# Kernel optimization log

Measured on AMD Instinct MI355X. Metric: run time of the kernel, lower is better.

## Reference

```python
import jax, jax.numpy as jnp
import numpy as np

J = 58        # n_joints (two 29-joint dancers)
NIN = 192     # n_in
H = 512       # n_hid
NOUT = 128    # n_out
B = 32        # batch


def _xavier(key, fan_in, fan_out):
    return jax.random.normal(key, (fan_in, fan_out), jnp.float32) * jnp.sqrt(2.0 / (fan_in + fan_out))


def setup_inputs() -> dict:
    key = jax.random.key(0)
    ks = jax.random.split(key, 8)
    # fully-connected directed graph, no self loops: E = J*(J-1) = 3306
    src_np, dst_np = np.nonzero(1 - np.eye(J, dtype=np.int32))
    edge_index = jnp.asarray(np.stack([src_np, dst_np]), dtype=jnp.int32)  # [2, E]
    x = jax.random.normal(ks[0], (B, 1, J, NIN), jnp.float32)
    return dict(
        x=x,
        edge_index=edge_index,
        gcn1_w=_xavier(ks[1], NIN, H), gcn1_b=jnp.full((H,), 0.1, jnp.float32),
        mlp1_w=_xavier(ks[2], 2 * H, H), mlp1_b=jnp.full((H,), 0.1, jnp.float32),
        bn1_g=jnp.ones((H,), jnp.float32), bn1_b=jnp.zeros((H,), jnp.float32),
        gcn2_w=_xavier(ks[3], H, H), gcn2_b=jnp.full((H,), 0.1, jnp.float32),
        mlp2_w=_xavier(ks[4], 3 * H, H), mlp2_b=jnp.full((H,), 0.1, jnp.float32),
        bn2_g=jnp.ones((H,), jnp.float32), bn2_b=jnp.zeros((H,), jnp.float32),
        fc_w=_xavier(ks[5], H, NOUT), fc_b=jnp.full((NOUT,), 0.1, jnp.float32),
    )


def _gcn_norm_adj(edge_index, n_nodes, dtype):
    # PyG GCNConv default: A_hat = A + I, sym-normalized D^-1/2 A_hat D^-1/2
    src, dst = edge_index[0], edge_index[1]
    adj = jnp.zeros((n_nodes, n_nodes), dtype).at[dst, src].add(1.0) + jnp.eye(n_nodes, dtype=dtype)
    d_inv_sqrt = 1.0 / jnp.sqrt(adj.sum(axis=1))
    return d_inv_sqrt[:, None] * adj * d_inv_sqrt[None, :]


def _batchnorm(h, gamma, beta):
    # BatchNorm1d (training-mode stats) over (batch, length) per channel
    mu = h.mean(axis=(0, 1))
    var = h.var(axis=(0, 1))
    return (h - mu) * jax.lax.rsqrt(var + 1e-5) * gamma + beta


def reference(x, edge_index, gcn1_w, gcn1_b, mlp1_w, mlp1_b, bn1_g, bn1_b,
              gcn2_w, gcn2_b, mlp2_w, mlp2_b, bn2_g, bn2_b, fc_w, fc_b):
    b = x.shape[0]
    n = x.shape[2]
    x = x.reshape(b, n, -1)                                  # [B, J, n_in]
    src, dst = edge_index[0], edge_index[1]
    A = _gcn_norm_adj(edge_index, n, x.dtype)                # [J, J]

    # GCNConv 1 + relu
    h = jax.nn.relu(jnp.einsum('ij,bjf->bif', A, x) @ gcn1_w + gcn1_b)   # [B, J, H]
    # node2edge: concat(sender, receiver) feats -> MLP1 -> BN (batched gather)
    e = jnp.concatenate([h[:, src], h[:, dst]], axis=-1)     # [B, E, 2H]
    e = jax.nn.relu(e @ mlp1_w + mlp1_b)                     # [B, E, H]
    e = _batchnorm(e, bn1_g, bn1_b)                          # dropout p=0 -> identity
    x_skip = e
    # edge2node: sum incoming edge feats per receiver node (m_in^T @ e)
    node = jnp.zeros((b, n, e.shape[-1]), e.dtype).at[:, dst].add(e)     # [B, J, H]

    # GCNConv 2 + relu
    h2 = jax.nn.relu(jnp.einsum('ij,bjf->bif', A, node) @ gcn2_w + gcn2_b)
    # node2edge again, concat skip, MLP2, BN, fc_out
    e2 = jnp.concatenate([h2[:, src], h2[:, dst], x_skip], axis=-1)      # [B, E, 3H]
    e2 = jax.nn.relu(e2 @ mlp2_w + mlp2_b)
    e2 = _batchnorm(e2, bn2_g, bn2_b)
    return e2 @ fc_w + fc_b                                  # [B, E, n_out]
```

## Files before the change

kernel.cpp:

```cpp
#include <hip/hip_runtime.h>
#include <stdint.h>

#define J_ 58
#define E_ 3306
#define B_ 32
#define NIN_ 192
#define H_ 512
#define NOUT_ 128
#define M_EDGE (B_*E_)
#define M_PAD  (M_EDGE + 64)
#define M_NODE (B_*J_)
#define NSLOT 64

typedef unsigned short u16;
typedef __attribute__((ext_vector_type(8))) short short8v;
typedef __attribute__((ext_vector_type(4))) float f32x4;

__device__ __forceinline__ float b2f(u16 u){ return __uint_as_float(((uint32_t)u)<<16); }
__device__ __forceinline__ u16 f2b(float f){
  uint32_t u = __float_as_uint(f);
  u += 0x7FFFu + ((u>>16)&1u);
  return (u16)(u>>16);
}
__device__ __forceinline__ void async16(const void* g, void* l){
  __builtin_amdgcn_global_load_lds((const __attribute__((address_space(1))) uint32_t*)g,
                                   (__attribute__((address_space(3))) uint32_t*)l, 16, 0, 0);
}

__global__ __launch_bounds__(256) void build_graph(const int* __restrict__ ei,
    float* __restrict__ Adj, float* __restrict__ aind,
    int* __restrict__ csroff, int* __restrict__ csredg)
{
  __shared__ float adj[J_][J_];
  __shared__ int   deg[J_];
  __shared__ float dinv[J_];
  __shared__ int   off[J_+1];
  __shared__ int   cur[J_];
  const int t = threadIdx.x;
  const int* srcI = ei;
  const int* dstI = ei + E_;
  for (int i = t; i < J_*J_; i += 256) adj[i/J_][i%J_] = 0.f;
  if (t < J_) { deg[t] = 0; cur[t] = 0; }
  __syncthreads();
  for (int e = t; e < E_; e += 256) {
    atomicAdd(&adj[dstI[e]][srcI[e]], 1.f);
    atomicAdd(&deg[dstI[e]], 1);
  }
  __syncthreads();
  if (t < J_) adj[t][t] += 1.f;
  __syncthreads();
  if (t < J_) {
    float s = 0.f;
    for (int j = 0; j < J_; ++j) s += adj[t][j];
    dinv[t] = rsqrtf(s);
  }
  __syncthreads();
  for (int i = t; i < J_*J_; i += 256) {
    int r = i / J_, c = i % J_;
    Adj[i] = dinv[r]*adj[r][c]*dinv[c];
  }
  if (t < J_) {
    float s = 0.f;
    for (int j = 0; j < J_; ++j) s += dinv[t]*adj[t][j]*dinv[j]*(float)deg[j];
    aind[t] = s;
  }
  if (t == 0) {
    off[0] = 0;
    for (int n = 0; n < J_; ++n) off[n+1] = off[n] + deg[n];
  }
  __syncthreads();
  if (t <= J_) csroff[t] = off[t];
  for (int e = t; e < E_; e += 256) {
    int d = dstI[e];
    int p = atomicAdd(&cur[d], 1);
    csredg[off[d] + p] = e;
  }
}

__global__ __launch_bounds__(256) void transpose_cv(const float* __restrict__ src,
    u16* __restrict__ dst, int K, int N)
{
  int idx = blockIdx.x*256 + threadIdx.x;
  if (idx >= K*N) return;
  int k = idx / N, n = idx - k*N;
  dst[(size_t)n*K + k] = f2b(src[idx]);
}

__global__ __launch_bounds__(192) void ax_kernel(const float* __restrict__ Adj,
    const float* __restrict__ x, u16* __restrict__ Ax)
{
  int bi = blockIdx.x;
  int b = bi / J_, i = bi - b*J_;
  __shared__ float Arow[J_];
  if (threadIdx.x < J_) Arow[threadIdx.x] = Adj[i*J_ + threadIdx.x];
  __syncthreads();
  int f = threadIdx.x;
  const float* xb = x + (size_t)b*J_*NIN_ + f;
  float acc = 0.f;
  for (int j = 0; j < J_; ++j) acc += Arow[j]*xb[(size_t)j*NIN_];
  Ax[(size_t)bi*NIN_ + f] = f2b(acc);
}

template<int MODE>
__global__ __launch_bounds__(256) void gemm64(
    const u16* __restrict__ Aop, const u16* __restrict__ Bt,
    const int M, const int N, const int K,
    const float* __restrict__ bias,
    u16* __restrict__ outB, float* __restrict__ outF)
{
  __shared__ __align__(16) u16 Al[64*32];
  __shared__ __align__(16) u16 Bl[64*32];
  const int tid = threadIdx.x;
  const int w = tid >> 6, l = tid & 63;
  const int row0 = blockIdx.x * 64, col0 = blockIdx.y * 64;
  f32x4 acc[4] = {};
  const u16* ag = Aop + (size_t)(row0 + (tid>>2))*K + (tid&3)*8;
  const u16* bg = Bt  + (size_t)(col0 + (tid>>2))*K + (tid&3)*8;
  const int fr = l & 15, fg = l >> 4;
  const int nk = K >> 5;
  for (int kt = 0; kt < nk; ++kt) {
    short8v av = *(const short8v*)ag;
    short8v bv = *(const short8v*)bg;
    ag += 32; bg += 32;
    __syncthreads();
    *(short8v*)(Al + tid*8) = av;
    *(short8v*)(Bl + tid*8) = bv;
    __syncthreads();
    short8v a = *(const short8v*)(Al + (w*16 + fr)*32 + fg*8);
#pragma unroll
    for (int nt = 0; nt < 4; ++nt) {
      short8v b = *(const short8v*)(Bl + (nt*16 + fr)*32 + fg*8);
      acc[nt] = __builtin_amdgcn_mfma_f32_16x16x32_bf16(a, b, acc[nt], 0, 0, 0);
    }
  }
#pragma unroll
  for (int nt = 0; nt < 4; ++nt) {
    int gc = col0 + nt*16 + fr;
    float bv = (MODE == 1) ? bias[gc] : 0.f;
#pragma unroll
    for (int r = 0; r < 4; ++r) {
      int gr = row0 + w*16 + fg*4 + r;
      if (MODE == 0) outF[(size_t)gr*N + gc] = acc[nt][r];
      else           outB[(size_t)gr*N + gc] = f2b(fmaxf(acc[nt][r] + bv, 0.f));
    }
  }
}

template<int MODE>
__global__ __launch_bounds__(256, 3) void gemm128(
    const u16* __restrict__ Aop, const u16* __restrict__ Bt,
    const int N, const int K,
    const float* __restrict__ g1, const float* __restrict__ g2,
    const float* __restrict__ crow,
    const int* __restrict__ srcI, const int* __restrict__ dstI,
    double* __restrict__ sumslot, double* __restrict__ sqslot,
    u16* __restrict__ outB, float* __restrict__ outF)
{
  __shared__ __align__(16) u16 Al[2][128*32];
  __shared__ __align__(16) u16 Bl[2][128*32];
  const int tid = threadIdx.x;
  const int w = tid >> 6, l = tid & 63;
  const int wm = w >> 1, wn = w & 1;
  const int row0 = blockIdx.x * 128, col0 = blockIdx.y * 128;
  const int fr = l & 15, fg = l >> 4;
  f32x4 acc[4][4] = {};
  const int srow = l >> 2, skoff = (l & 3) * 8;
  const u16* agA = Aop + (size_t)(row0 + w*16 + srow)*K + skoff;
  const u16* agB = Bt  + (size_t)(col0 + w*16 + srow)*K + skoff;
  const size_t rstep = (size_t)64 * K;
  const int nk = K >> 5;
  async16(agA,         &Al[0][w*512]);
  async16(agA + rstep, &Al[0][2048 + w*512]);
  async16(agB,         &Bl[0][w*512]);
  async16(agB + rstep, &Bl[0][2048 + w*512]);
  __syncthreads();
  for (int kt = 0; kt < nk; ++kt) {
    const int cur = kt & 1, nxt = cur ^ 1;
    if (kt + 1 < nk) {
      const u16* pa = agA + (kt+1)*32;
      const u16* pb = agB + (kt+1)*32;
      async16(pa,         &Al[nxt][w*512]);
      async16(pa + rstep, &Al[nxt][2048 + w*512]);
      async16(pb,         &Bl[nxt][w*512]);
      async16(pb + rstep, &Bl[nxt][2048 + w*512]);
    }
    short8v a[4], b[4];
#pragma unroll
    for (int i = 0; i < 4; ++i)
      a[i] = *(const short8v*)(&Al[cur][(wm*64 + i*16 + fr)*32 + fg*8]);
#pragma unroll
    for (int j = 0; j < 4; ++j)
      b[j] = *(const short8v*)(&Bl[cur][(wn*64 + j*16 + fr)*32 + fg*8]);
#pragma unroll
    for (int i = 0; i < 4; ++i)
#pragma unroll
      for (int j = 0; j < 4; ++j)
        acc[i][j] = __builtin_amdgcn_mfma_f32_16x16x32_bf16(a[i], b[j], acc[i][j], 0, 0, 0);
    __syncthreads();
  }

  if (MODE == 2) {
    int mr[4][4];
    uint32_t off1[4][4], off2[4][4];
#pragma unroll
    for (int i = 0; i < 4; ++i)
#pragma unroll
      for (int r = 0; r < 4; ++r) {
        int m = row0 + wm*64 + i*16 + fg*4 + r;
        mr[i][r] = m;
        int mm = (m < M_EDGE) ? m : 0;
        uint32_t bb = (uint32_t)mm / E_;
        uint32_t ke = (uint32_t)mm - bb*E_;
        off1[i][r] = (bb*J_ + (uint32_t)srcI[ke])*H_;
        off2[i][r] = (bb*J_ + (uint32_t)dstI[ke])*H_;
      }
    const int slot = blockIdx.x & (NSLOT-1);
#pragma unroll
    for (int j = 0; j < 4; ++j) {
      int gc = col0 + wn*64 + j*16 + fr;
      float cr = crow[gc];
      double s = 0.0, q = 0.0;
#pragma unroll
      for (int i = 0; i < 4; ++i)
#pragma unroll
        for (int r = 0; r < 4; ++r) {
          float v = acc[i][j][r] + g1[off1[i][r] + gc] + g2[off2[i][r] + gc] + cr;
          v = fmaxf(v, 0.f);
          if (mr[i][r] < M_EDGE) {
            outB[(size_t)mr[i][r]*N + gc] = f2b(v);
            double vd = (double)v;
            s += vd; q += vd*vd;
          }
        }
      s += __shfl_xor(s, 16); s += __shfl_xor(s, 32);
      q += __shfl_xor(q, 16); q += __shfl_xor(q, 32);
      if (fg == 0) {
        atomicAdd(&sumslot[(size_t)slot*H_ + gc], s);
        atomicAdd(&sqslot [(size_t)slot*H_ + gc], q);
      }
    }
  } else {
#pragma unroll
    for (int j = 0; j < 4; ++j) {
      int gc = col0 + wn*64 + j*16 + fr;
      float cr = crow[gc];
#pragma unroll
      for (int i = 0; i < 4; ++i)
#pragma unroll
        for (int r = 0; r < 4; ++r) {
          int m = row0 + wm*64 + i*16 + fg*4 + r;
          if (m < M_EDGE) outF[(size_t)m*N + gc] = acc[i][j][r] + cr;
        }
    }
  }
}

__global__ __launch_bounds__(256) void edge1_kernel(const float* __restrict__ hs,
    const float* __restrict__ hd, const float* __restrict__ b1,
    const int* __restrict__ srcI, const int* __restrict__ dstI,
    u16* __restrict__ e_raw, double* __restrict__ sumslot, double* __restrict__ sqslot)
{
  const int t = threadIdx.x;
  const int row0 = blockIdx.x * 16;
  float bv0 = b1[t], bv1 = b1[t+256];
  double s0=0.0,q0=0.0,s1=0.0,q1=0.0;
  for (int r = 0; r < 16; ++r) {
    int m = row0 + r;
    uint32_t bb = (uint32_t)m / E_;
    uint32_t ke = (uint32_t)m - bb*E_;
    const float* ps = hs + ((size_t)bb*J_ + srcI[ke])*H_;
    const float* pd = hd + ((size_t)bb*J_ + dstI[ke])*H_;
    float v0 = fmaxf(ps[t]     + pd[t]     + bv0, 0.f);
    float v1 = fmaxf(ps[t+256] + pd[t+256] + bv1, 0.f);
    e_raw[(size_t)m*H_ + t]       = f2b(v0);
    e_raw[(size_t)m*H_ + t + 256] = f2b(v1);
    double d0 = (double)v0, d1 = (double)v1;
    s0 += d0; q0 += d0*d0; s1 += d1; q1 += d1*d1;
  }
  const int slot = blockIdx.x & (NSLOT-1);
  atomicAdd(&sumslot[(size_t)slot*H_ + t],     s0);
  atomicAdd(&sumslot[(size_t)slot*H_ + t+256], s1);
  atomicAdd(&sqslot [(size_t)slot*H_ + t],     q0);
  atomicAdd(&sqslot [(size_t)slot*H_ + t+256], q1);
}

__global__ __launch_bounds__(512) void bn_fin(const double* __restrict__ sumslot,
    const double* __restrict__ sqslot, const float* __restrict__ g, const float* __restrict__ b,
    float* __restrict__ scale, float* __restrict__ shift)
{
  int c = threadIdx.x;
  double s = 0.0, q = 0.0;
  for (int k = 0; k < NSLOT; ++k) { s += sumslot[(size_t)k*H_ + c]; q += sqslot[(size_t)k*H_ + c]; }
  const double invM = 1.0 / (double)M_EDGE;
  double mu = s * invM;
  double var = q * invM - mu*mu;
  if (var < 0.0) var = 0.0;
  float sc = g[c] * (float)(1.0 / sqrt(var + 1e-5));
  scale[c] = sc;
  shift[c] = b[c] - (float)mu*sc;
}

__global__ __launch_bounds__(256) void build_wc(const float* __restrict__ m2w,
    const float* __restrict__ m2b, const float* __restrict__ scale1, const float* __restrict__ shift1,
    u16* __restrict__ WcT, float* __restrict__ crow)
{
  int n = blockIdx.x;
  int t = threadIdx.x;
  __shared__ float red[256];
  float part = 0.f;
  for (int k = t; k < H_; k += 256) {
    float wv = m2w[(size_t)(2*H_ + k)*H_ + n];
    WcT[(size_t)n*H_ + k] = f2b(scale1[k]*wv);
    part += shift1[k]*wv;
  }
  red[t] = part; __syncthreads();
  for (int s = 128; s; s >>= 1) { if (t < s) red[t] += red[t+s]; __syncthreads(); }
  if (t == 0) crow[n] = red[0] + m2b[n];
}

__global__ __launch_bounds__(256) void build_fc(const float* __restrict__ fcw,
    const float* __restrict__ fcb, const float* __restrict__ scale2, const float* __restrict__ shift2,
    u16* __restrict__ fcT, float* __restrict__ cvec)
{
  int n = blockIdx.x;
  int t = threadIdx.x;
  __shared__ float red[256];
  float part = 0.f;
  for (int k = t; k < H_; k += 256) {
    float wv = fcw[(size_t)k*NOUT_ + n];
    fcT[(size_t)n*H_ + k] = f2b(scale2[k]*wv);
    part += shift2[k]*wv;
  }
  red[t] = part; __syncthreads();
  for (int s = 128; s; s >>= 1) { if (t < s) red[t] += red[t+s]; __syncthreads(); }
  if (t == 0) cvec[n] = red[0] + fcb[n];
}

__global__ __launch_bounds__(256) void scatter_kernel(const u16* __restrict__ e_raw,
    const int* __restrict__ csroff, const int* __restrict__ csredg, float* __restrict__ node_raw)
{
  int bi = blockIdx.x;
  int b = bi / J_, n = bi - b*J_;
  int beg = csroff[n], end = csroff[n+1];
  int c0 = threadIdx.x, c1 = threadIdx.x + 256;
  float a0 = 0.f, a1 = 0.f;
  for (int p = beg; p < end; ++p) {
    const u16* er = e_raw + ((size_t)b*E_ + csredg[p])*H_;
    a0 += b2f(er[c0]); a1 += b2f(er[c1]);
  }
  node_raw[(size_t)bi*H_ + c0] = a0;
  node_raw[(size_t)bi*H_ + c1] = a1;
}

__global__ __launch_bounds__(256) void an_kernel(const float* __restrict__ Adj,
    const float* __restrict__ node_raw, const float* __restrict__ scale1,
    const float* __restrict__ shift1, const float* __restrict__ aind, u16* __restrict__ An)
{
  int bi = blockIdx.x;
  int b = bi / J_, i = bi - b*J_;
  __shared__ float Arow[J_];
  if (threadIdx.x < J_) Arow[threadIdx.x] = Adj[i*J_ + threadIdx.x];
  __syncthreads();
  float ai = aind[i];
#pragma unroll
  for (int h = 0; h < 2; ++h) {
    int c = threadIdx.x + h*256;
    const float* nb = node_raw + (size_t)b*J_*H_ + c;
    float acc = 0.f;
    for (int j = 0; j < J_; ++j) acc += Arow[j]*nb[(size_t)j*H_];
    An[(size_t)bi*H_ + c] = f2b(scale1[c]*acc + shift1[c]*ai);
  }
}

extern "C" void kernel_launch(void* const* d_in, const int* in_sizes, int n_in,
                              void* d_out, int out_size, void* d_ws, size_t ws_size,
                              hipStream_t stream)
{
  const float* x    = (const float*)d_in[0];
  const int*   ei   = (const int*)d_in[1];
  const float* g1w  = (const float*)d_in[2];
  const float* g1b  = (const float*)d_in[3];
  const float* m1w  = (const float*)d_in[4];
  const float* m1b  = (const float*)d_in[5];
  const float* bn1g = (const float*)d_in[6];
  const float* bn1b = (const float*)d_in[7];
  const float* g2w  = (const float*)d_in[8];
  const float* g2b  = (const float*)d_in[9];
  const float* m2w  = (const float*)d_in[10];
  const float* m2b  = (const float*)d_in[11];
  const float* bn2g = (const float*)d_in[12];
  const float* bn2b = (const float*)d_in[13];
  const float* fcw  = (const float*)d_in[14];
  const float* fcb  = (const float*)d_in[15];

  char* wsp = (char*)d_ws;
  size_t off = 0;
  auto alloc = [&](size_t bytes) -> char* {
    char* p = wsp + off;
    off = (off + bytes + 255) & ~(size_t)255;
    return p;
  };
  float* Adj    = (float*)alloc(J_*J_*4);
  float* aind   = (float*)alloc(J_*4);
  int*   csroff = (int*)alloc((J_+1)*4);
  int*   csredg = (int*)alloc(E_*4);
  float* scale1 = (float*)alloc(H_*4);
  float* shift1 = (float*)alloc(H_*4);
  float* scale2 = (float*)alloc(H_*4);
  float* shift2 = (float*)alloc(H_*4);
  float* crow1  = (float*)alloc(H_*4);
  float* cvec   = (float*)alloc(NOUT_*4);
  double* slots = (double*)alloc((size_t)4*NSLOT*H_*8);
  double* sum1 = slots;
  double* sq1  = slots + (size_t)NSLOT*H_;
  double* sum2 = slots + (size_t)2*NSLOT*H_;
  double* sq2  = slots + (size_t)3*NSLOT*H_;
  u16* g1T  = (u16*)alloc((size_t)H_*NIN_*2);
  u16* g2T  = (u16*)alloc((size_t)H_*H_*2);
  u16* W1aT = (u16*)alloc((size_t)H_*H_*2);
  u16* W1bT = (u16*)alloc((size_t)H_*H_*2);
  u16* W2aT = (u16*)alloc((size_t)H_*H_*2);
  u16* W2bT = (u16*)alloc((size_t)H_*H_*2);
  u16* WcT  = (u16*)alloc((size_t)H_*H_*2);
  u16* fcT  = (u16*)alloc((size_t)NOUT_*H_*2);
  u16* Ax   = (u16*)alloc((size_t)M_NODE*NIN_*2);
  u16* h    = (u16*)alloc((size_t)M_NODE*H_*2);
  float* hs = (float*)alloc((size_t)M_NODE*H_*4);
  float* hd = (float*)alloc((size_t)M_NODE*H_*4);
  float* node_raw = (float*)alloc((size_t)M_NODE*H_*4);
  u16* An   = (u16*)alloc((size_t)M_NODE*H_*2);
  u16* h2   = (u16*)alloc((size_t)M_NODE*H_*2);
  float* h2s = (float*)alloc((size_t)M_NODE*H_*4);
  float* h2d = (float*)alloc((size_t)M_NODE*H_*4);
  u16* e_raw = (u16*)alloc((size_t)M_PAD*H_*2);
  u16* e2    = (u16*)alloc((size_t)M_PAD*H_*2);
  if (off > ws_size) return;

  const int* srcI = ei;
  const int* dstI = ei + E_;
  float* outF = (float*)d_out;

  hipMemsetAsync(slots, 0, (size_t)4*NSLOT*H_*8, stream);
  build_graph<<<1, 256, 0, stream>>>(ei, Adj, aind, csroff, csredg);

  transpose_cv<<<(NIN_*H_+255)/256, 256, 0, stream>>>(g1w, g1T, NIN_, H_);
  transpose_cv<<<(H_*H_+255)/256, 256, 0, stream>>>(g2w, g2T, H_, H_);
  transpose_cv<<<(H_*H_+255)/256, 256, 0, stream>>>(m1w, W1aT, H_, H_);
  transpose_cv<<<(H_*H_+255)/256, 256, 0, stream>>>(m1w + (size_t)H_*H_, W1bT, H_, H_);
  transpose_cv<<<(H_*H_+255)/256, 256, 0, stream>>>(m2w, W2aT, H_, H_);
  transpose_cv<<<(H_*H_+255)/256, 256, 0, stream>>>(m2w + (size_t)H_*H_, W2bT, H_, H_);

  ax_kernel<<<M_NODE, 192, 0, stream>>>(Adj, x, Ax);

  gemm64<1><<<dim3(M_NODE/64, H_/64), 256, 0, stream>>>(Ax, g1T, M_NODE, H_, NIN_,
      g1b, h, nullptr);
  gemm64<0><<<dim3(M_NODE/64, H_/64), 256, 0, stream>>>(h, W1aT, M_NODE, H_, H_,
      nullptr, nullptr, hs);
  gemm64<0><<<dim3(M_NODE/64, H_/64), 256, 0, stream>>>(h, W1bT, M_NODE, H_, H_,
      nullptr, nullptr, hd);
  edge1_kernel<<<M_EDGE/16, 256, 0, stream>>>(hs, hd, m1b, srcI, dstI, e_raw, sum1, sq1);
  bn_fin<<<1, 512, 0, stream>>>(sum1, sq1, bn1g, bn1b, scale1, shift1);
  build_wc<<<H_, 256, 0, stream>>>(m2w, m2b, scale1, shift1, WcT, crow1);
  scatter_kernel<<<M_NODE, 256, 0, stream>>>(e_raw, csroff, csredg, node_raw);
  an_kernel<<<M_NODE, 256, 0, stream>>>(Adj, node_raw, scale1, shift1, aind, An);
  gemm64<1><<<dim3(M_NODE/64, H_/64), 256, 0, stream>>>(An, g2T, M_NODE, H_, H_,
      g2b, h2, nullptr);
  gemm64<0><<<dim3(M_NODE/64, H_/64), 256, 0, stream>>>(h2, W2aT, M_NODE, H_, H_,
      nullptr, nullptr, h2s);
  gemm64<0><<<dim3(M_NODE/64, H_/64), 256, 0, stream>>>(h2, W2bT, M_NODE, H_, H_,
      nullptr, nullptr, h2d);
  gemm128<2><<<dim3(M_PAD/128, H_/128), 256, 0, stream>>>(e_raw, WcT, H_, H_,
      h2s, h2d, crow1, srcI, dstI, sum2, sq2, e2, nullptr);
  bn_fin<<<1, 512, 0, stream>>>(sum2, sq2, bn2g, bn2b, scale2, shift2);
  build_fc<<<NOUT_, 256, 0, stream>>>(fcw, fcb, scale2, shift2, fcT, cvec);
  gemm128<3><<<dim3(M_PAD/128, NOUT_/128), 256, 0, stream>>>(e2, fcT, NOUT_, H_,
      nullptr, nullptr, cvec, nullptr, nullptr, nullptr, nullptr, nullptr, outF);
}
```

Before: 500.1 us.

## Triple-buffer gemm128 loads and merge paired sender/receiver GEMMs into one

Result: no change. 491.0 us (-1.8%).

```diff
diff --git a/kernel.cpp b/kernel.cpp
--- a/kernel.cpp
+++ b/kernel.cpp
@@ -84,6 +84,16 @@
   if (idx >= K*N) return;
   int k = idx / N, n = idx - k*N;
   dst[(size_t)n*K + k] = f2b(src[idx]);
+}
+
+__global__ __launch_bounds__(256) void transpose_pair(const float* __restrict__ src,
+    u16* __restrict__ dst)
+{
+  int idx = blockIdx.x*256 + threadIdx.x;
+  if (idx >= 2*H_*H_) return;
+  int np = idx / H_, k = idx - np*H_;
+  float v = (np < H_) ? src[(size_t)k*H_ + np] : src[(size_t)(H_+k)*H_ + (np-H_)];
+  dst[idx] = f2b(v);
 }
 
 __global__ __launch_bounds__(192) void ax_kernel(const float* __restrict__ Adj,
@@ -150,14 +160,14 @@
 __global__ __launch_bounds__(256, 3) void gemm128(
     const u16* __restrict__ Aop, const u16* __restrict__ Bt,
     const int N, const int K,
-    const float* __restrict__ g1, const float* __restrict__ g2,
+    const float* __restrict__ gsd,
     const float* __restrict__ crow,
     const int* __restrict__ srcI, const int* __restrict__ dstI,
     double* __restrict__ sumslot, double* __restrict__ sqslot,
     u16* __restrict__ outB, float* __restrict__ outF)
 {
-  __shared__ __align__(16) u16 Al[2][128*32];
-  __shared__ __align__(16) u16 Bl[2][128*32];
+  __shared__ __align__(16) u16 Al[3*128*32];
+  __shared__ __align__(16) u16 Bl[3*128*32];
   const int tid = threadIdx.x;
   const int w = tid >> 6, l = tid & 63;
   const int wm = w >> 1, wn = w & 1;
@@ -169,34 +179,46 @@
   const u16* agB = Bt  + (size_t)(col0 + w*16 + srow)*K + skoff;
   const size_t rstep = (size_t)64 * K;
   const int nk = K >> 5;
-  async16(agA,         &Al[0][w*512]);
-  async16(agA + rstep, &Al[0][2048 + w*512]);
-  async16(agB,         &Bl[0][w*512]);
-  async16(agB + rstep, &Bl[0][2048 + w*512]);
-  __syncthreads();
+  async16(agA,          Al + w*512);
+  async16(agA + rstep,  Al + 2048 + w*512);
+  async16(agB,          Bl + w*512);
+  async16(agB + rstep,  Bl + 2048 + w*512);
+  async16(agA + 32,         Al + 4096 + w*512);
+  async16(agA + 32 + rstep, Al + 4096 + 2048 + w*512);
+  async16(agB + 32,         Bl + 4096 + w*512);
+  async16(agB + 32 + rstep, Bl + 4096 + 2048 + w*512);
+  int cur = 0;
+  int pfb = 2;
   for (int kt = 0; kt < nk; ++kt) {
-    const int cur = kt & 1, nxt = cur ^ 1;
-    if (kt + 1 < nk) {
-      const u16* pa = agA + (kt+1)*32;
-      const u16* pb = agB + (kt+1)*32;
-      async16(pa,         &Al[nxt][w*512]);
-      async16(pa + rstep, &Al[nxt][2048 + w*512]);
-      async16(pb,         &Bl[nxt][w*512]);
-      async16(pb + rstep, &Bl[nxt][2048 + w*512]);
+    if (kt + 1 < nk) asm volatile("s_waitcnt vmcnt(4)" ::: "memory");
+    else             asm volatile("s_waitcnt vmcnt(0)" ::: "memory");
+    asm volatile("s_barrier" ::: "memory");
+    if (kt + 2 < nk) {
+      const u16* pa = agA + (size_t)(kt+2)*32;
+      const u16* pb = agB + (size_t)(kt+2)*32;
+      u16* A0 = Al + pfb*4096;
+      u16* B0 = Bl + pfb*4096;
+      async16(pa,         A0 + w*512);
+      async16(pa + rstep, A0 + 2048 + w*512);
+      async16(pb,         B0 + w*512);
+      async16(pb + rstep, B0 + 2048 + w*512);
     }
+    const u16* Ac = Al + cur*4096;
+    const u16* Bc = Bl + cur*4096;
     short8v a[4], b[4];
 #pragma unroll
     for (int i = 0; i < 4; ++i)
-      a[i] = *(const short8v*)(&Al[cur][(wm*64 + i*16 + fr)*32 + fg*8]);
+      a[i] = *(const short8v*)(Ac + (wm*64 + i*16 + fr)*32 + fg*8);
 #pragma unroll
     for (int j = 0; j < 4; ++j)
-      b[j] = *(const short8v*)(&Bl[cur][(wn*64 + j*16 + fr)*32 + fg*8]);
+      b[j] = *(const short8v*)(Bc + (wn*64 + j*16 + fr)*32 + fg*8);
 #pragma unroll
     for (int i = 0; i < 4; ++i)
 #pragma unroll
       for (int j = 0; j < 4; ++j)
         acc[i][j] = __builtin_amdgcn_mfma_f32_16x16x32_bf16(a[i], b[j], acc[i][j], 0, 0, 0);
-    __syncthreads();
+    cur = (cur == 2) ? 0 : cur + 1;
+    pfb = (pfb == 2) ? 0 : pfb + 1;
   }
 
   if (MODE == 2) {
@@ -211,8 +233,8 @@
         int mm = (m < M_EDGE) ? m : 0;
         uint32_t bb = (uint32_t)mm / E_;
         uint32_t ke = (uint32_t)mm - bb*E_;
-        off1[i][r] = (bb*J_ + (uint32_t)srcI[ke])*H_;
-        off2[i][r] = (bb*J_ + (uint32_t)dstI[ke])*H_;
+        off1[i][r] = (bb*J_ + (uint32_t)srcI[ke])*1024u;
+        off2[i][r] = (bb*J_ + (uint32_t)dstI[ke])*1024u + 512u;
       }
     const int slot = blockIdx.x & (NSLOT-1);
 #pragma unroll
@@ -224,7 +246,7 @@
       for (int i = 0; i < 4; ++i)
 #pragma unroll
         for (int r = 0; r < 4; ++r) {
-          float v = acc[i][j][r] + g1[off1[i][r] + gc] + g2[off2[i][r] + gc] + cr;
+          float v = acc[i][j][r] + gsd[off1[i][r] + gc] + gsd[off2[i][r] + gc] + cr;
           v = fmaxf(v, 0.f);
           if (mr[i][r] < M_EDGE) {
             outB[(size_t)mr[i][r]*N + gc] = f2b(v);
@@ -255,8 +277,8 @@
   }
 }
 
-__global__ __launch_bounds__(256) void edge1_kernel(const float* __restrict__ hs,
-    const float* __restrict__ hd, const float* __restrict__ b1,
+__global__ __launch_bounds__(256) void edge1_kernel(const float* __restrict__ hsd,
+    const float* __restrict__ b1,
     const int* __restrict__ srcI, const int* __restrict__ dstI,
     u16* __restrict__ e_raw, double* __restrict__ sumslot, double* __restrict__ sqslot)
 {
@@ -268,8 +290,8 @@
     int m = row0 + r;
     uint32_t bb = (uint32_t)m / E_;
     uint32_t ke = (uint32_t)m - bb*E_;
-    const float* ps = hs + ((size_t)bb*J_ + srcI[ke])*H_;
-    const float* pd = hd + ((size_t)bb*J_ + dstI[ke])*H_;
+    const float* ps = hsd + ((size_t)bb*J_ + srcI[ke])*1024;
+    const float* pd = hsd + ((size_t)bb*J_ + dstI[ke])*1024 + 512;
     float v0 = fmaxf(ps[t]     + pd[t]     + bv0, 0.f);
     float v1 = fmaxf(ps[t+256] + pd[t+256] + bv1, 0.f);
     e_raw[(size_t)m*H_ + t]       = f2b(v0);
@@ -415,23 +437,19 @@
   double* sq1  = slots + (size_t)NSLOT*H_;
   double* sum2 = slots + (size_t)2*NSLOT*H_;
   double* sq2  = slots + (size_t)3*NSLOT*H_;
-  u16* g1T  = (u16*)alloc((size_t)H_*NIN_*2);
-  u16* g2T  = (u16*)alloc((size_t)H_*H_*2);
-  u16* W1aT = (u16*)alloc((size_t)H_*H_*2);
-  u16* W1bT = (u16*)alloc((size_t)H_*H_*2);
-  u16* W2aT = (u16*)alloc((size_t)H_*H_*2);
-  u16* W2bT = (u16*)alloc((size_t)H_*H_*2);
-  u16* WcT  = (u16*)alloc((size_t)H_*H_*2);
-  u16* fcT  = (u16*)alloc((size_t)NOUT_*H_*2);
-  u16* Ax   = (u16*)alloc((size_t)M_NODE*NIN_*2);
-  u16* h    = (u16*)alloc((size_t)M_NODE*H_*2);
-  float* hs = (float*)alloc((size_t)M_NODE*H_*4);
-  float* hd = (float*)alloc((size_t)M_NODE*H_*4);
+  u16* g1T   = (u16*)alloc((size_t)H_*NIN_*2);
+  u16* g2T   = (u16*)alloc((size_t)H_*H_*2);
+  u16* W1abT = (u16*)alloc((size_t)2*H_*H_*2);
+  u16* W2abT = (u16*)alloc((size_t)2*H_*H_*2);
+  u16* WcT   = (u16*)alloc((size_t)H_*H_*2);
+  u16* fcT   = (u16*)alloc((size_t)NOUT_*H_*2);
+  u16* Ax    = (u16*)alloc((size_t)M_NODE*NIN_*2);
+  u16* h     = (u16*)alloc((size_t)M_NODE*H_*2);
+  float* hsd  = (float*)alloc((size_t)M_NODE*2*H_*4);
   float* node_raw = (float*)alloc((size_t)M_NODE*H_*4);
-  u16* An   = (u16*)alloc((size_t)M_NODE*H_*2);
-  u16* h2   = (u16*)alloc((size_t)M_NODE*H_*2);
-  float* h2s = (float*)alloc((size_t)M_NODE*H_*4);
-  float* h2d = (float*)alloc((size_t)M_NODE*H_*4);
+  u16* An    = (u16*)alloc((size_t)M_NODE*H_*2);
+  u16* h2    = (u16*)alloc((size_t)M_NODE*H_*2);
+  float* h2sd = (float*)alloc((size_t)M_NODE*2*H_*4);
   u16* e_raw = (u16*)alloc((size_t)M_PAD*H_*2);
   u16* e2    = (u16*)alloc((size_t)M_PAD*H_*2);
   if (off > ws_size) return;
@@ -445,34 +463,28 @@
 
   transpose_cv<<<(NIN_*H_+255)/256, 256, 0, stream>>>(g1w, g1T, NIN_, H_);
   transpose_cv<<<(H_*H_+255)/256, 256, 0, stream>>>(g2w, g2T, H_, H_);
-  transpose_cv<<<(H_*H_+255)/256, 256, 0, stream>>>(m1w, W1aT, H_, H_);
-  transpose_cv<<<(H_*H_+255)/256, 256, 0, stream>>>(m1w + (size_t)H_*H_, W1bT, H_, H_);
-  transpose_cv<<<(H_*H_+255)/256, 256, 0, stream>>>(m2w, W2aT, H_, H_);
-  transpose_cv<<<(H_*H_+255)/256, 256, 0, stream>>>(m2w + (size_t)H_*H_, W2bT, H_, H_);
+  transpose_pair<<<(2*H_*H_+255)/256, 256, 0, stream>>>(m1w, W1abT);
+  transpose_pair<<<(2*H_*H_+255)/256, 256, 0, stream>>>(m2w, W2abT);
 
   ax_kernel<<<M_NODE, 192, 0, stream>>>(Adj, x, Ax);
 
   gemm64<1><<<dim3(M_NODE/64, H_/64), 256, 0, stream>>>(Ax, g1T, M_NODE, H_, NIN_,
       g1b, h, nullptr);
-  gemm64<0><<<dim3(M_NODE/64, H_/64), 256, 0, stream>>>(h, W1aT, M_NODE, H_, H_,
-      nullptr, nullptr, hs);
-  gemm64<0><<<dim3(M_NODE/64, H_/64), 256, 0, stream>>>(h, W1bT, M_NODE, H_, H_,
-      nullptr, nullptr, hd);
-  edge1_kernel<<<M_EDGE/16, 256, 0, stream>>>(hs, hd, m1b, srcI, dstI, e_raw, sum1, sq1);
+  gemm64<0><<<dim3(M_NODE/64, 2*H_/64), 256, 0, stream>>>(h, W1abT, M_NODE, 2*H_, H_,
+      nullptr, nullptr, hsd);
+  edge1_kernel<<<M_EDGE/16, 256, 0, stream>>>(hsd, m1b, srcI, dstI, e_raw, sum1, sq1);
   bn_fin<<<1, 512, 0, stream>>>(sum1, sq1, bn1g, bn1b, scale1, shift1);
   build_wc<<<H_, 256, 0, stream>>>(m2w, m2b, scale1, shift1, WcT, crow1);
   scatter_kernel<<<M_NODE, 256, 0, stream>>>(e_raw, csroff, csredg, node_raw);
   an_kernel<<<M_NODE, 256, 0, stream>>>(Adj, node_raw, scale1, shift1, aind, An);
   gemm64<1><<<dim3(M_NODE/64, H_/64), 256, 0, stream>>>(An, g2T, M_NODE, H_, H_,
       g2b, h2, nullptr);
-  gemm64<0><<<dim3(M_NODE/64, H_/64), 256, 0, stream>>>(h2, W2aT, M_NODE, H_, H_,
-      nullptr, nullptr, h2s);
-  gemm64<0><<<dim3(M_NODE/64, H_/64), 256, 0, stream>>>(h2, W2bT, M_NODE, H_, H_,
-      nullptr, nullptr, h2d);
+  gemm64<0><<<dim3(M_NODE/64, 2*H_/64), 256, 0, stream>>>(h2, W2abT, M_NODE, 2*H_, H_,
+      nullptr, nullptr, h2sd);
   gemm128<2><<<dim3(M_PAD/128, H_/128), 256, 0, stream>>>(e_raw, WcT, H_, H_,
-      h2s, h2d, crow1, srcI, dstI, sum2, sq2, e2, nullptr);
+      h2sd, crow1, srcI, dstI, sum2, sq2, e2, nullptr);
   bn_fin<<<1, 512, 0, stream>>>(sum2, sq2, bn2g, bn2b, scale2, shift2);
   build_fc<<<NOUT_, 256, 0, stream>>>(fcw, fcb, scale2, shift2, fcT, cvec);
   gemm128<3><<<dim3(M_PAD/128, NOUT_/128), 256, 0, stream>>>(e2, fcT, NOUT_, H_,
-      nullptr, nullptr, cvec, nullptr, nullptr, nullptr, nullptr, nullptr, outF);
-}
+      nullptr, cvec, nullptr, nullptr, nullptr, nullptr, nullptr, outF);
+}
```
